# Kernel tuning notes

Hardware: AMD Instinct MI355X
Metric: run time of the kernel (lower is better)

## Reference

```python
import jax, jax.numpy as jnp
import numpy as np

N = 100000   # nodes (single ntype)
R = 3        # relations
E = 500000   # edges per relation
H = 4        # attention heads
F = 64       # out_feat per head
IN = 256     # in_feat
NEG_SLOPE = 0.2  # DGL GATConv default


def setup_inputs() -> dict:
    key = jax.random.key(0)
    ks = jax.random.split(key, 7)
    x = jax.random.normal(ks[0], (N, IN), jnp.float32)
    src = jax.random.randint(ks[1], (R, E), 0, N, dtype=jnp.int32)
    dst = jax.random.randint(ks[2], (R, E), 0, N, dtype=jnp.int32)
    W = jax.random.normal(ks[3], (R, IN, H * F), jnp.float32) / np.sqrt(IN).astype(np.float32)
    attn_l = jax.random.normal(ks[4], (R, H, F), jnp.float32) * 0.1
    attn_r = jax.random.normal(ks[5], (R, H, F), jnp.float32) * 0.1
    bias = jnp.zeros((R, H * F), jnp.float32)
    return {"x": x, "W": W, "attn_l": attn_l, "attn_r": attn_r, "bias": bias,
            "src": src, "dst": dst}


def _gat_relation(x, W_r, al_r, ar_r, b_r, src_r, dst_r):
    # projection: [N, H, F]
    z = (x @ W_r).reshape(N, H, F)
    # per-node attention logits: [N, H]
    el = jnp.sum(z * al_r, axis=-1)
    er = jnp.sum(z * ar_r, axis=-1)
    # edge scores: [E, H]
    e = jax.nn.leaky_relu(el[src_r] + er[dst_r], negative_slope=NEG_SLOPE)
    # segment softmax over incoming edges of each dst node
    m = jax.ops.segment_max(e, dst_r, num_segments=N)      # [N, H]
    ee = jnp.exp(e - m[dst_r])                              # [E, H]
    den = jax.ops.segment_sum(ee, dst_r, num_segments=N)   # [N, H]
    alpha = ee / den[dst_r]                                 # [E, H]
    # weighted scatter-aggregate: [N, H, F]
    rst = jax.ops.segment_sum(z[src_r] * alpha[:, :, None], dst_r, num_segments=N)
    return rst + b_r.reshape(1, H, F)


def reference(x, W, attn_l, attn_r, bias, src, dst):
    # HeteroGraphConv aggregates relations targeting the same ntype with 'sum'
    out = jnp.zeros((N, H, F), x.dtype)
    for r in range(R):
        out = out + _gat_relation(x, W[r], attn_l[r], attn_r[r], bias[r], src[r], dst[r])
    # RelGATConvLayer._apply: activation(h.view(-1, out_feat*num_heads)); dropout=0
    return jax.nn.elu(out.reshape(N, H * F))
```

## Files before the change

### kernel.cpp

```cpp
#include <hip/hip_runtime.h>
#include <hip/hip_bf16.h>


#define RN 100000
#define RE 500000
#define RH 4
#define RIN 256
#define RR 3
#define RHF 256
#define NE3 (RR * RE)
#define N3  (RR * RN)

typedef __attribute__((ext_vector_type(8))) short short8;
typedef __attribute__((ext_vector_type(4))) float f32x4;

static __device__ __forceinline__ float b2f(unsigned short u) {
  return __uint_as_float(((unsigned int)u) << 16);
}
static __device__ __forceinline__ unsigned short f2b(float f) {
  unsigned int u = __float_as_uint(f);
  u += 0x7FFF + ((u >> 16) & 1);
  return (unsigned short)(u >> 16);
}

__global__ __launch_bounds__(256) void rgat_convx(
    const float* __restrict__ x, unsigned short* __restrict__ xb) {
  const size_t i = ((size_t)blockIdx.x * 256 + threadIdx.x) * 4;
  if (i >= (size_t)RN * RIN) return;
  const float4 v = *(const float4*)(x + i);
  ushort4 o;
  o.x = f2b(v.x); o.y = f2b(v.y); o.z = f2b(v.z); o.w = f2b(v.w);
  *(ushort4*)(xb + i) = o;
}

__global__ __launch_bounds__(256) void rgat_convw(
    const float* __restrict__ W, unsigned short* __restrict__ wbt) {
  const int o = blockIdx.x * 256 + threadIdx.x;
  if (o >= RR * RIN * RHF) return;
  const int r = o / (RIN * RHF);
  const int rem = o - r * (RIN * RHF);
  const int n = rem >> 8;
  const int k = rem & 255;
  wbt[o] = f2b(W[r * (RIN * RHF) + k * RHF + n]);
}

__global__ __launch_bounds__(256) void rgat_gemm_bf16(
    const unsigned short* __restrict__ xb, const unsigned short* __restrict__ wbt,
    unsigned short* __restrict__ zb, const float* __restrict__ al,
    const float* __restrict__ ar, float* __restrict__ el,
    float* __restrict__ er) {
  __shared__ unsigned short As[128 * 32];
  __shared__ unsigned short Bs[128 * 32];
  const int tid = threadIdx.x;
  const int lane = tid & 63, wid = tid >> 6;
  const int wr = wid >> 1, wc = wid & 1;
  const int m0 = blockIdx.x * 128;
  const int n0 = blockIdx.y * 128;
  const int r  = blockIdx.z;

  f32x4 acc[4][4] = {};
  const unsigned short* Bbase = wbt + (size_t)r * (RIN * RHF);

  for (int k0 = 0; k0 < RIN; k0 += 32) {
#pragma unroll
    for (int i = 0; i < 2; ++i) {
      const int c = wid * 128 + i * 64 + lane;
      const int row = c >> 2, c4 = c & 3;
      const unsigned short* ga = xb + (size_t)(m0 + row) * RIN + k0 + c4 * 8;
      __builtin_amdgcn_global_load_lds(
          (const __attribute__((address_space(1))) void*)ga,
          (__attribute__((address_space(3))) void*)(As + (wid * 128 + i * 64) * 8),
          16, 0, 0);
      const unsigned short* gb = Bbase + (size_t)(n0 + row) * RIN + k0 + c4 * 8;
      __builtin_amdgcn_global_load_lds(
          (const __attribute__((address_space(1))) void*)gb,
          (__attribute__((address_space(3))) void*)(Bs + (wid * 128 + i * 64) * 8),
          16, 0, 0);
    }
    asm volatile("s_waitcnt vmcnt(0)" ::: "memory");
    __syncthreads();

    short8 af[4], bfr[4];
#pragma unroll
    for (int mi = 0; mi < 4; ++mi)
      af[mi] = *(const short8*)(As + ((wr * 64 + mi * 16 + (lane & 15)) * 32 + (lane >> 4) * 8));
#pragma unroll
    for (int ni = 0; ni < 4; ++ni)
      bfr[ni] = *(const short8*)(Bs + ((wc * 64 + ni * 16 + (lane & 15)) * 32 + (lane >> 4) * 8));
#pragma unroll
    for (int mi = 0; mi < 4; ++mi)
#pragma unroll
      for (int ni = 0; ni < 4; ++ni)
        acc[mi][ni] = __builtin_amdgcn_mfma_f32_16x16x32_bf16(af[mi], bfr[ni], acc[mi][ni], 0, 0, 0);
    __syncthreads();
  }

  const int head = blockIdx.y * 2 + wc;
  float alv[4], arv[4];
#pragma unroll
  for (int ni = 0; ni < 4; ++ni) {
    alv[ni] = al[r * RHF + head * 64 + ni * 16 + (lane & 15)];
    arv[ni] = ar[r * RHF + head * 64 + ni * 16 + (lane & 15)];
  }

  const int mbase = m0 + wr * 64;
#pragma unroll
  for (int mi = 0; mi < 4; ++mi) {
#pragma unroll
    for (int q = 0; q < 4; ++q) {
      const int m = mbase + mi * 16 + (lane >> 4) * 4 + q;
      float pl = 0.f, pr = 0.f;
#pragma unroll
      for (int ni = 0; ni < 4; ++ni) {
        pl += acc[mi][ni][q] * alv[ni];
        pr += acc[mi][ni][q] * arv[ni];
      }
#pragma unroll
      for (int off = 1; off < 16; off <<= 1) {
        pl += __shfl_xor(pl, off);
        pr += __shfl_xor(pr, off);
      }
      if (m < RN) {
        if ((lane & 15) == 0) {
          el[(size_t)(r * (size_t)RN + m) * RH + head] = pl;
          er[(size_t)(r * (size_t)RN + m) * RH + head] = pr;
        }
        unsigned short* zrow = zb + (size_t)r * ((size_t)RN * RHF) + (size_t)m * RHF
                               + n0 + wc * 64 + (lane & 15);
#pragma unroll
        for (int ni = 0; ni < 4; ++ni) zrow[ni * 16] = f2b(acc[mi][ni][q]);
      }
    }
  }
}

__global__ __launch_bounds__(256) void rgat_hist(
    const int* __restrict__ dst, int* __restrict__ deg2) {
  const int i = blockIdx.x * 256 + threadIdx.x;
  if (i >= NE3) return;
  const int r = i / RE;
  atomicAdd(&deg2[dst[i] * RR + r], 1);
}

__global__ __launch_bounds__(256) void rgat_scan1(
    const int* __restrict__ deg, int* __restrict__ offs, int* __restrict__ bsum) {
  __shared__ int sh[256];
  const int tid = threadIdx.x;
  const int base = blockIdx.x * 1024 + tid * 4;
  int v[4]; int s = 0;
#pragma unroll
  for (int j = 0; j < 4; ++j) {
    v[j] = (base + j < N3) ? deg[base + j] : 0;
    s += v[j];
  }
  sh[tid] = s;
  __syncthreads();
  for (int off = 1; off < 256; off <<= 1) {
    int t = (tid >= off) ? sh[tid - off] : 0;
    __syncthreads();
    sh[tid] += t;
    __syncthreads();
  }
  int run = sh[tid] - s;
  if (tid == 255) bsum[blockIdx.x] = sh[255];
#pragma unroll
  for (int j = 0; j < 4; ++j) {
    if (base + j < N3) offs[base + j] = run;
    run += v[j];
  }
}

__global__ __launch_bounds__(512) void rgat_scan2(int* __restrict__ bsum, int nb) {
  __shared__ int sh[512];
  const int tid = threadIdx.x;
  const int v = (tid < nb) ? bsum[tid] : 0;
  sh[tid] = v;
  __syncthreads();
  for (int off = 1; off < 512; off <<= 1) {
    int t = (tid >= off) ? sh[tid - off] : 0;
    __syncthreads();
    sh[tid] += t;
    __syncthreads();
  }
  if (tid < nb) bsum[tid] = sh[tid] - v;
}

__global__ __launch_bounds__(256) void rgat_scan3(
    int* __restrict__ offs, const int* __restrict__ bsum) {
  const int base = blockIdx.x * 1024 + threadIdx.x * 4;
  const int b = bsum[blockIdx.x];
#pragma unroll
  for (int j = 0; j < 4; ++j)
    if (base + j < N3) offs[base + j] += b;
}

__global__ __launch_bounds__(256) void rgat_scatter(
    const int* __restrict__ src, const int* __restrict__ dst,
    const float* __restrict__ el, const float* __restrict__ er,
    int* __restrict__ offs2, int* __restrict__ csrc,
    float4* __restrict__ cee) {
  const int i = blockIdx.x * 256 + threadIdx.x;
  if (i >= NE3) return;
  const int r = i / RE;
  const int s = src[i];
  const int d = dst[i];
  const int pos = atomicAdd(&offs2[d * RR + r], 1);
  const float4 elv = *(const float4*)(el + (size_t)(r * (size_t)RN + s) * RH);
  const float4 erv = *(const float4*)(er + (size_t)(r * (size_t)RN + d) * RH);
  float e0 = elv.x + erv.x, e1 = elv.y + erv.y, e2 = elv.z + erv.z, e3 = elv.w + erv.w;
  e0 = e0 > 0.f ? e0 : 0.2f * e0;
  e1 = e1 > 0.f ? e1 : 0.2f * e1;
  e2 = e2 > 0.f ? e2 : 0.2f * e2;
  e3 = e3 > 0.f ? e3 : 0.2f * e3;
  csrc[pos] = s;
  cee[pos] = make_float4(__expf(e0), __expf(e1), __expf(e2), __expf(e3));
}

__global__ __launch_bounds__(256) void rgat_aggregate(
    const unsigned short* __restrict__ zb, const int* __restrict__ csrc,
    const float* __restrict__ ceef, const int* __restrict__ deg2,
    const int* __restrict__ offs2, const float* __restrict__ bias,
    float* __restrict__ out) {
  __shared__ float shn[4][RR][RHF];
  __shared__ float shd[4][RR][RH];
  const int n = blockIdx.x;
  const int tid = threadIdx.x;
  const int wid = tid >> 6, lane = tid & 63;
  const int hw = tid >> 5;
  const int sub = lane & 31;
  const int h = sub >> 3;
  const int c = sub * 8;

  float accr[RR][8];
  float denr[RR];
#pragma unroll
  for (int r = 0; r < RR; ++r) {
    denr[r] = 0.f;
#pragma unroll
    for (int k = 0; k < 8; ++k) accr[r][k] = 0.f;
  }

#pragma unroll
  for (int r = 0; r < RR; ++r) {
    const int key = n * RR + r;
    const int dr = deg2[key];
    const int end = offs2[key];
    const int start = end - dr;
    const unsigned short* zB = zb + (size_t)r * ((size_t)RN * RHF) + c;
    for (int t = hw; t < dr; t += 8) {
      const int p = start + t;
      const int s = csrc[p];
      const float a = ceef[p * 4 + h];
      const short8 zv = *(const short8*)(zB + (size_t)s * RHF);
      denr[r] += a;
#pragma unroll
      for (int k = 0; k < 8; ++k)
        accr[r][k] += a * b2f((unsigned short)zv[k]);
    }
  }

#pragma unroll
  for (int r = 0; r < RR; ++r) {
    denr[r] += __shfl_xor(denr[r], 32);
#pragma unroll
    for (int k = 0; k < 8; ++k) accr[r][k] += __shfl_xor(accr[r][k], 32);
  }

  if (lane < 32) {
#pragma unroll
    for (int r = 0; r < RR; ++r) {
      *(float4*)&shn[wid][r][c] = make_float4(accr[r][0], accr[r][1], accr[r][2], accr[r][3]);
      *(float4*)&shn[wid][r][c + 4] = make_float4(accr[r][4], accr[r][5], accr[r][6], accr[r][7]);
      if ((sub & 7) == 0) shd[wid][r][h] = denr[r];
    }
  }
  __syncthreads();

  const int col = tid;
  const int hh = col >> 6;
  float v = bias[col] + bias[RHF + col] + bias[2 * RHF + col];
#pragma unroll
  for (int r = 0; r < RR; ++r) {
    const float dn = shd[0][r][hh] + shd[1][r][hh] + shd[2][r][hh] + shd[3][r][hh];
    const float nm = shn[0][r][col] + shn[1][r][col] + shn[2][r][col] + shn[3][r][col];
    v += (dn > 0.f) ? nm / dn : 0.f;
  }
  v = v > 0.f ? v : (__expf(v) - 1.f);
  out[(size_t)n * RHF + col] = v;
}

extern "C" void kernel_launch(void* const* d_in, const int* in_sizes, int n_in,
                              void* d_out, int out_size, void* d_ws, size_t ws_size,
                              hipStream_t stream) {
  const float* x    = (const float*)d_in[0];
  const float* W    = (const float*)d_in[1];
  const float* al   = (const float*)d_in[2];
  const float* ar   = (const float*)d_in[3];
  const float* bias = (const float*)d_in[4];
  const int*   src  = (const int*)d_in[5];
  const int*   dst  = (const int*)d_in[6];
  float* out = (float*)d_out;

  char* p = (char*)d_ws;
  unsigned short* xb  = (unsigned short*)p; p += (size_t)RN * RIN * 2;
  unsigned short* wbt = (unsigned short*)p; p += (size_t)RR * RIN * RHF * 2;
  unsigned short* zb  = (unsigned short*)p; p += (size_t)RR * RN * RHF * 2;
  float* el    = (float*)p;  p += (size_t)RR * RN * RH * 4;
  float* er    = (float*)p;  p += (size_t)RR * RN * RH * 4;
  int* deg2    = (int*)p;    p += (size_t)N3 * 4;
  int* offs2   = (int*)p;    p += (size_t)N3 * 4;
  int* csrc    = (int*)p;    p += (size_t)NE3 * 4;
  float4* cee  = (float4*)p; p += (size_t)NE3 * 16;
  int* bsum    = (int*)p;    p += 2048;

  const int NB1 = (N3 + 1023) / 1024;

  hipMemsetAsync(deg2, 0, (size_t)N3 * 4, stream);

  rgat_convx<<<(RN * RIN / 4 + 255) / 256, 256, 0, stream>>>(x, xb);
  rgat_convw<<<(RR * RIN * RHF + 255) / 256, 256, 0, stream>>>(W, wbt);

  rgat_hist<<<(NE3 + 255) / 256, 256, 0, stream>>>(dst, deg2);
  rgat_scan1<<<NB1, 256, 0, stream>>>(deg2, offs2, bsum);
  rgat_scan2<<<1, 512, 0, stream>>>(bsum, NB1);
  rgat_scan3<<<NB1, 256, 0, stream>>>(offs2, bsum);

  rgat_gemm_bf16<<<dim3((RN + 127) / 128, RHF / 128, RR), 256, 0, stream>>>(
      xb, wbt, zb, al, ar, el, er);

  rgat_scatter<<<(NE3 + 255) / 256, 256, 0, stream>>>(src, dst, el, er, offs2,
                                                      csrc, cee);

  rgat_aggregate<<<RN, 256, 0, stream>>>(zb, csrc, (const float*)cee, deg2,
                                         offs2, bias, out);
}
```

Measured before the change: 677.3 us.

## Precompute softmax denominators in scatter and restructure aggregate with batched gathers

The scatter kernel now accumulates the per-destination, per-relation, per-head softmax denominators with float atomics, so aggregation can normalize each edge weight up front. Aggregation drops the per-relation accumulators and the denominator reduction, and sums all relations into one 4-float accumulator per lane. Each wave handles one edge at a time, with lanes covering all 256 columns, and issues 4 independent gathers per iteration to keep more memory requests in flight. The cost is 4 extra float atomics per edge in scatter and a larger memset. Float atomics also make the summation order nondeterministic.

```diff
diff --git a/kernel.cpp b/kernel.cpp
--- a/kernel.cpp
+++ b/kernel.cpp
@@ -198,13 +198,14 @@
     const int* __restrict__ src, const int* __restrict__ dst,
     const float* __restrict__ el, const float* __restrict__ er,
     int* __restrict__ offs2, int* __restrict__ csrc,
-    float4* __restrict__ cee) {
+    float4* __restrict__ cee, float* __restrict__ den) {
   const int i = blockIdx.x * 256 + threadIdx.x;
   if (i >= NE3) return;
   const int r = i / RE;
   const int s = src[i];
   const int d = dst[i];
-  const int pos = atomicAdd(&offs2[d * RR + r], 1);
+  const int key = d * RR + r;
+  const int pos = atomicAdd(&offs2[key], 1);
   const float4 elv = *(const float4*)(el + (size_t)(r * (size_t)RN + s) * RH);
   const float4 erv = *(const float4*)(er + (size_t)(r * (size_t)RN + d) * RH);
   float e0 = elv.x + erv.x, e1 = elv.y + erv.y, e2 = elv.z + erv.z, e3 = elv.w + erv.w;
@@ -212,79 +213,74 @@
   e1 = e1 > 0.f ? e1 : 0.2f * e1;
   e2 = e2 > 0.f ? e2 : 0.2f * e2;
   e3 = e3 > 0.f ? e3 : 0.2f * e3;
+  const float p0 = __expf(e0), p1 = __expf(e1), p2 = __expf(e2), p3 = __expf(e3);
   csrc[pos] = s;
-  cee[pos] = make_float4(__expf(e0), __expf(e1), __expf(e2), __expf(e3));
+  cee[pos] = make_float4(p0, p1, p2, p3);
+  float* dn = den + (size_t)key * RH;
+  atomicAdd(&dn[0], p0);
+  atomicAdd(&dn[1], p1);
+  atomicAdd(&dn[2], p2);
+  atomicAdd(&dn[3], p3);
 }
 
 __global__ __launch_bounds__(256) void rgat_aggregate(
     const unsigned short* __restrict__ zb, const int* __restrict__ csrc,
     const float* __restrict__ ceef, const int* __restrict__ deg2,
-    const int* __restrict__ offs2, const float* __restrict__ bias,
-    float* __restrict__ out) {
-  __shared__ float shn[4][RR][RHF];
-  __shared__ float shd[4][RR][RH];
+    const int* __restrict__ offs2, const float* __restrict__ den,
+    const float* __restrict__ bias, float* __restrict__ out) {
+  __shared__ float shn[4][RHF];
   const int n = blockIdx.x;
   const int tid = threadIdx.x;
   const int wid = tid >> 6, lane = tid & 63;
-  const int hw = tid >> 5;
-  const int sub = lane & 31;
-  const int h = sub >> 3;
-  const int c = sub * 8;
-
-  float accr[RR][8];
-  float denr[RR];
-#pragma unroll
-  for (int r = 0; r < RR; ++r) {
-    denr[r] = 0.f;
-#pragma unroll
-    for (int k = 0; k < 8; ++k) accr[r][k] = 0.f;
-  }
+  const int h = lane >> 4;
+  const int c = lane * 4;
+
+  float a0 = 0.f, a1 = 0.f, a2 = 0.f, a3 = 0.f;
 
 #pragma unroll
   for (int r = 0; r < RR; ++r) {
     const int key = n * RR + r;
     const int dr = deg2[key];
-    const int end = offs2[key];
-    const int start = end - dr;
+    const int start = offs2[key] - dr;
+    const float dn = den[(size_t)key * RH + h];
+    const float inv = (dn > 0.f) ? 1.f / dn : 0.f;
     const unsigned short* zB = zb + (size_t)r * ((size_t)RN * RHF) + c;
-    for (int t = hw; t < dr; t += 8) {
-      const int p = start + t;
-      const int s = csrc[p];
-      const float a = ceef[p * 4 + h];
-      const short8 zv = *(const short8*)(zB + (size_t)s * RHF);
-      denr[r] += a;
-#pragma unroll
-      for (int k = 0; k < 8; ++k)
-        accr[r][k] += a * b2f((unsigned short)zv[k]);
+    for (int base = wid; base < dr; base += 16) {
+      int ss[4];
+      float aa[4];
+      ushort4 zv[4];
+#pragma unroll
+      for (int j = 0; j < 4; ++j) {
+        const int t = base + j * 4;
+        if (t < dr) {
+          const int p = start + t;
+          ss[j] = csrc[p];
+          aa[j] = ceef[p * 4 + h];
+        } else {
+          ss[j] = -1;
+        }
+      }
+#pragma unroll
+      for (int j = 0; j < 4; ++j)
+        if (ss[j] >= 0) zv[j] = *(const ushort4*)(zB + (size_t)ss[j] * RHF);
+#pragma unroll
+      for (int j = 0; j < 4; ++j) {
+        if (ss[j] < 0) continue;
+        const float a = aa[j] * inv;
+        a0 += a * b2f(zv[j].x);
+        a1 += a * b2f(zv[j].y);
+        a2 += a * b2f(zv[j].z);
+        a3 += a * b2f(zv[j].w);
+      }
     }
   }
 
-#pragma unroll
-  for (int r = 0; r < RR; ++r) {
-    denr[r] += __shfl_xor(denr[r], 32);
-#pragma unroll
-    for (int k = 0; k < 8; ++k) accr[r][k] += __shfl_xor(accr[r][k], 32);
-  }
-
-  if (lane < 32) {
-#pragma unroll
-    for (int r = 0; r < RR; ++r) {
-      *(float4*)&shn[wid][r][c] = make_float4(accr[r][0], accr[r][1], accr[r][2], accr[r][3]);
-      *(float4*)&shn[wid][r][c + 4] = make_float4(accr[r][4], accr[r][5], accr[r][6], accr[r][7]);
-      if ((sub & 7) == 0) shd[wid][r][h] = denr[r];
-    }
-  }
+  *(float4*)&shn[wid][c] = make_float4(a0, a1, a2, a3);
   __syncthreads();
 
   const int col = tid;
-  const int hh = col >> 6;
-  float v = bias[col] + bias[RHF + col] + bias[2 * RHF + col];
-#pragma unroll
-  for (int r = 0; r < RR; ++r) {
-    const float dn = shd[0][r][hh] + shd[1][r][hh] + shd[2][r][hh] + shd[3][r][hh];
-    const float nm = shn[0][r][col] + shn[1][r][col] + shn[2][r][col] + shn[3][r][col];
-    v += (dn > 0.f) ? nm / dn : 0.f;
-  }
+  float v = shn[0][col] + shn[1][col] + shn[2][col] + shn[3][col]
+          + bias[col] + bias[RHF + col] + bias[2 * RHF + col];
   v = v > 0.f ? v : (__expf(v) - 1.f);
   out[(size_t)n * RHF + col] = v;
 }
@@ -308,6 +304,7 @@
   float* el    = (float*)p;  p += (size_t)RR * RN * RH * 4;
   float* er    = (float*)p;  p += (size_t)RR * RN * RH * 4;
   int* deg2    = (int*)p;    p += (size_t)N3 * 4;
+  float* den   = (float*)p;  p += (size_t)N3 * RH * 4;
   int* offs2   = (int*)p;    p += (size_t)N3 * 4;
   int* csrc    = (int*)p;    p += (size_t)NE3 * 4;
   float4* cee  = (float4*)p; p += (size_t)NE3 * 16;
@@ -315,7 +312,7 @@
 
   const int NB1 = (N3 + 1023) / 1024;
 
-  hipMemsetAsync(deg2, 0, (size_t)N3 * 4, stream);
+  hipMemsetAsync(deg2, 0, (size_t)N3 * 4 + (size_t)N3 * RH * 4, stream);
 
   rgat_convx<<<(RN * RIN / 4 + 255) / 256, 256, 0, stream>>>(x, xb);
   rgat_convw<<<(RR * RIN * RHF + 255) / 256, 256, 0, stream>>>(W, wbt);
@@ -329,8 +326,8 @@
       xb, wbt, zb, al, ar, el, er);
 
   rgat_scatter<<<(NE3 + 255) / 256, 256, 0, stream>>>(src, dst, el, er, offs2,
-                                                      csrc, cee);
+                                                      csrc, cee, den);
 
   rgat_aggregate<<<RN, 256, 0, stream>>>(zb, csrc, (const float*)cee, deg2,
-                                         offs2, bias, out);
-}
+                                         offs2, den, bias, out);
+}
```

After: 964.5 us. +42.4%, slower.

## Precompute softmax inverse denominators and batch gathers in aggregate

Applied to the files above, without the earlier changes.

Adds a separate per-(node,relation) kernel that sums the exp scores and stores inverse denominators. The aggregate kernel then needs one accumulator set instead of one per relation. Each half-wave now issues four independent neighbor gathers before accumulating, which raises memory-level parallelism and lowers register use. The cost is an extra kernel launch and a second pass over the edge score array.

```diff
diff --git a/kernel.cpp b/kernel.cpp
--- a/kernel.cpp
+++ b/kernel.cpp
@@ -216,75 +216,89 @@
   cee[pos] = make_float4(__expf(e0), __expf(e1), __expf(e2), __expf(e3));
 }
 
+__global__ __launch_bounds__(256) void rgat_den(
+    const float4* __restrict__ cee, const int* __restrict__ deg2,
+    const int* __restrict__ offs2, float* __restrict__ invd) {
+  const int key = blockIdx.x * 256 + threadIdx.x;
+  if (key >= N3) return;
+  const int d = deg2[key];
+  const int end = offs2[key];
+  float s0 = 0.f, s1 = 0.f, s2 = 0.f, s3 = 0.f;
+  for (int p = end - d; p < end; ++p) {
+    const float4 v = cee[p];
+    s0 += v.x; s1 += v.y; s2 += v.z; s3 += v.w;
+  }
+  float4 o;
+  o.x = s0 > 0.f ? 1.f / s0 : 0.f;
+  o.y = s1 > 0.f ? 1.f / s1 : 0.f;
+  o.z = s2 > 0.f ? 1.f / s2 : 0.f;
+  o.w = s3 > 0.f ? 1.f / s3 : 0.f;
+  *(float4*)(invd + (size_t)key * RH) = o;
+}
+
 __global__ __launch_bounds__(256) void rgat_aggregate(
     const unsigned short* __restrict__ zb, const int* __restrict__ csrc,
     const float* __restrict__ ceef, const int* __restrict__ deg2,
-    const int* __restrict__ offs2, const float* __restrict__ bias,
-    float* __restrict__ out) {
-  __shared__ float shn[4][RR][RHF];
-  __shared__ float shd[4][RR][RH];
+    const int* __restrict__ offs2, const float* __restrict__ invd,
+    const float* __restrict__ bias, float* __restrict__ out) {
+  __shared__ float shn[4][RHF];
   const int n = blockIdx.x;
   const int tid = threadIdx.x;
   const int wid = tid >> 6, lane = tid & 63;
-  const int hw = tid >> 5;
+  const int hw = lane >> 5;
   const int sub = lane & 31;
   const int h = sub >> 3;
   const int c = sub * 8;
 
-  float accr[RR][8];
-  float denr[RR];
-#pragma unroll
-  for (int r = 0; r < RR; ++r) {
-    denr[r] = 0.f;
-#pragma unroll
-    for (int k = 0; k < 8; ++k) accr[r][k] = 0.f;
-  }
+  float acc[8] = {};
 
 #pragma unroll
   for (int r = 0; r < RR; ++r) {
     const int key = n * RR + r;
     const int dr = deg2[key];
-    const int end = offs2[key];
-    const int start = end - dr;
+    const int start = offs2[key] - dr;
+    const float inv = invd[(size_t)key * RH + h];
     const unsigned short* zB = zb + (size_t)r * ((size_t)RN * RHF) + c;
-    for (int t = hw; t < dr; t += 8) {
-      const int p = start + t;
-      const int s = csrc[p];
-      const float a = ceef[p * 4 + h];
-      const short8 zv = *(const short8*)(zB + (size_t)s * RHF);
-      denr[r] += a;
-#pragma unroll
-      for (int k = 0; k < 8; ++k)
-        accr[r][k] += a * b2f((unsigned short)zv[k]);
+    for (int base = wid * 8; base < dr; base += 32) {
+      int ss[4]; float aa[4];
+#pragma unroll
+      for (int j = 0; j < 4; ++j) {
+        const int t = base + j * 2 + hw;
+        if (t < dr) {
+          const int p = start + t;
+          ss[j] = csrc[p];
+          aa[j] = ceef[p * 4 + h];
+        } else {
+          ss[j] = 0;
+          aa[j] = 0.f;
+        }
+      }
+      short8 zv[4];
+#pragma unroll
+      for (int j = 0; j < 4; ++j)
+        zv[j] = *(const short8*)(zB + (size_t)ss[j] * RHF);
+#pragma unroll
+      for (int j = 0; j < 4; ++j) {
+        const float a = aa[j] * inv;
+#pragma unroll
+        for (int k = 0; k < 8; ++k)
+          acc[k] += a * b2f((unsigned short)zv[j][k]);
+      }
     }
   }
 
 #pragma unroll
-  for (int r = 0; r < RR; ++r) {
-    denr[r] += __shfl_xor(denr[r], 32);
-#pragma unroll
-    for (int k = 0; k < 8; ++k) accr[r][k] += __shfl_xor(accr[r][k], 32);
-  }
+  for (int k = 0; k < 8; ++k) acc[k] += __shfl_xor(acc[k], 32);
 
   if (lane < 32) {
-#pragma unroll
-    for (int r = 0; r < RR; ++r) {
-      *(float4*)&shn[wid][r][c] = make_float4(accr[r][0], accr[r][1], accr[r][2], accr[r][3]);
-      *(float4*)&shn[wid][r][c + 4] = make_float4(accr[r][4], accr[r][5], accr[r][6], accr[r][7]);
-      if ((sub & 7) == 0) shd[wid][r][h] = denr[r];
-    }
+    *(float4*)&shn[wid][c]     = make_float4(acc[0], acc[1], acc[2], acc[3]);
+    *(float4*)&shn[wid][c + 4] = make_float4(acc[4], acc[5], acc[6], acc[7]);
   }
   __syncthreads();
 
   const int col = tid;
-  const int hh = col >> 6;
-  float v = bias[col] + bias[RHF + col] + bias[2 * RHF + col];
-#pragma unroll
-  for (int r = 0; r < RR; ++r) {
-    const float dn = shd[0][r][hh] + shd[1][r][hh] + shd[2][r][hh] + shd[3][r][hh];
-    const float nm = shn[0][r][col] + shn[1][r][col] + shn[2][r][col] + shn[3][r][col];
-    v += (dn > 0.f) ? nm / dn : 0.f;
-  }
+  float v = shn[0][col] + shn[1][col] + shn[2][col] + shn[3][col]
+          + bias[col] + bias[RHF + col] + bias[2 * RHF + col];
   v = v > 0.f ? v : (__expf(v) - 1.f);
   out[(size_t)n * RHF + col] = v;
 }
@@ -308,6 +322,7 @@
   float* el    = (float*)p;  p += (size_t)RR * RN * RH * 4;
   float* er    = (float*)p;  p += (size_t)RR * RN * RH * 4;
   int* deg2    = (int*)p;    p += (size_t)N3 * 4;
+  float* invd  = (float*)p;  p += (size_t)N3 * RH * 4;
   int* offs2   = (int*)p;    p += (size_t)N3 * 4;
   int* csrc    = (int*)p;    p += (size_t)NE3 * 4;
   float4* cee  = (float4*)p; p += (size_t)NE3 * 16;
@@ -331,6 +346,8 @@
   rgat_scatter<<<(NE3 + 255) / 256, 256, 0, stream>>>(src, dst, el, er, offs2,
                                                       csrc, cee);
 
+  rgat_den<<<(N3 + 255) / 256, 256, 0, stream>>>(cee, deg2, offs2, invd);
+
   rgat_aggregate<<<RN, 256, 0, stream>>>(zb, csrc, (const float*)cee, deg2,
-                                         offs2, bias, out);
-}
+                                         offs2, invd, bias, out);
+}
```

Measured after the change: 740.8 us. 9.4% more time.
